# Kernel optimization log

Hardware: AMD Instinct MI355X
Metric: run time of the kernel (lower is better)

Reference implementation:

```python
import jax, jax.numpy as jnp
import numpy as np

DIM = 128
LAYER_GNN = 3
LAYER_CNN = 3
WINDOW = 11
K = 2 * WINDOW + 1  # conv kernel size 23
N_FP = 100000
N_WORD = 10000
N_ATOMS = 8192
L_PROT = 8192


def setup_inputs() -> dict:
    key = jax.random.key(0)
    ks = jax.random.split(key, 12)
    s = 0.1
    # sparse binary molecular adjacency (avg degree ~16), math is still dense matmul
    adjacency = (jax.random.uniform(ks[2], (N_ATOMS, N_ATOMS)) < 0.002).astype(jnp.float32)
    return {
        "fingerprints": jax.random.randint(ks[0], (N_ATOMS,), 0, N_FP),
        "words": jax.random.randint(ks[1], (L_PROT,), 0, N_WORD),
        "adjacency": adjacency,
        "emb_fp": jax.random.normal(ks[3], (N_FP, DIM), jnp.float32) * s,
        "emb_word": jax.random.normal(ks[4], (N_WORD, DIM), jnp.float32) * s,
        "Wg": jax.random.normal(ks[5], (LAYER_GNN, DIM, DIM), jnp.float32) * s,
        "bg": jnp.zeros((LAYER_GNN, DIM), jnp.float32),
        "conv_w": jax.random.normal(ks[6], (LAYER_CNN, 1, 1, K, K), jnp.float32) * s,
        "conv_b": jnp.zeros((LAYER_CNN,), jnp.float32),
        "Wa": jax.random.normal(ks[7], (DIM, DIM), jnp.float32) * s,
        "ba": jnp.zeros((DIM,), jnp.float32),
        "Wo": jax.random.normal(ks[8], (2, 2 * DIM), jnp.float32) * s,
        "bo": jnp.zeros((2,), jnp.float32),
    }


def reference(fingerprints, words, adjacency, emb_fp, emb_word, Wg, bg,
              conv_w, conv_b, Wa, ba, Wo, bo):
    # ---- GNN over compound graph ----
    xs = emb_fp[fingerprints]                      # [N_ATOMS, DIM]
    for i in range(LAYER_GNN):
        hs = jax.nn.relu(xs @ Wg[i].T + bg[i])     # Linear + ReLU
        xs = xs + adjacency @ hs                   # adjacency message passing
    x_compound = jnp.sum(xs, axis=0, keepdims=True)  # [1, DIM]

    # ---- attention-CNN over protein words ----
    xs_p = emb_word[words]                         # [L_PROT, DIM]
    x = x_compound                                 # [1, DIM]
    for i in range(LAYER_CNN):
        img = xs_p[None, None]                     # [1,1,L,DIM]
        h = jax.lax.conv_general_dilated(
            img, conv_w[i], window_strides=(1, 1),
            padding=[(WINDOW, WINDOW), (WINDOW, WINDOW)],
            dimension_numbers=("NCHW", "OIHW", "NCHW"))
        hs = jax.nn.relu(h[0, 0] + conv_b[i])      # [L, DIM]
        x = jax.nn.relu(x @ Wa.T + ba)             # [1, DIM]
        hs = jax.nn.relu(hs @ Wa.T + ba)           # [L, DIM]
        weights = jnp.tanh(x @ hs.T)               # [1, L]
        xs_p = weights.T * hs                      # [L, DIM]
    x_protein = jnp.sum(xs_p, axis=0, keepdims=True)  # [1, DIM]

    y = jnp.concatenate([x_compound, x_protein], axis=1)  # [1, 2*DIM]
    z = jax.nn.softmax(y @ Wo.T + bo, axis=1)
    return z[0]  # [2]
```

## Files before the change

kernel.cpp:

```cpp
#include <hip/hip_runtime.h>
#include <math.h>

#define DIM 128
#define NA 8192
#define CAP 64
#define NF (NA*DIM)

__global__ __launch_bounds__(256) void k_prep(
    const int* __restrict__ fp, const int* __restrict__ words,
    const float* __restrict__ emb_fp, const float* __restrict__ emb_w,
    const float* __restrict__ Wg, const float* __restrict__ Wa,
    float* __restrict__ xs, float* __restrict__ xsp,
    float* __restrict__ WgT, float* __restrict__ WaT,
    float* __restrict__ xc, float* __restrict__ xp,
    int* __restrict__ degcol, int* __restrict__ ctrs) {
  int b = blockIdx.x, tid = threadIdx.x;
  if (b < 1024) {
    int i = b * 256 + tid;
    int row = i >> 5, c4 = i & 31;
    ((float4*)(xs + (size_t)row * DIM))[c4] =
        ((const float4*)(emb_fp + (size_t)fp[row] * DIM))[c4];
  } else if (b < 2048) {
    int i = (b - 1024) * 256 + tid;
    int row = i >> 5, c4 = i & 31;
    ((float4*)(xsp + (size_t)row * DIM))[c4] =
        ((const float4*)(emb_w + (size_t)words[row] * DIM))[c4];
  } else if (b < 2112) {
    __shared__ float tile[32][33];
    int sub = b - 2048;
    int m = sub >> 4, t = sub & 15;
    int tx = t & 3, ty = t >> 2;
    const float* src = (m < 3) ? Wg + m * DIM * DIM : Wa;
    float*       dst = (m < 3) ? WgT + m * DIM * DIM : WaT;
    int x = tid & 31, y0 = tid >> 5;
    int xg = tx * 32 + x;
    for (int i = y0; i < 32; i += 8)
      tile[i][x] = src[(ty * 32 + i) * DIM + xg];
    __syncthreads();
    int xo = ty * 32 + x;
    for (int i = y0; i < 32; i += 8)
      dst[(tx * 32 + i) * DIM + xo] = tile[x][i];
  } else if (b == 2112) {
    if (tid < DIM) { xc[tid] = 0.f; xp[tid] = 0.f; }
    if (tid == 0) { ctrs[0] = 0; ctrs[1] = 0; }
  } else {
    int i = (b - 2113) * 256 + tid;
    int4 z; z.x = 0; z.y = 0; z.z = 0; z.w = 0;
    ((int4*)degcol)[i] = z;
  }
}

__global__ __launch_bounds__(512) void k_scan(
    const float* __restrict__ adj,
    const float* __restrict__ WgT, const float* __restrict__ bg,
    const float* __restrict__ xs, float* __restrict__ hs0,
    const float* __restrict__ xsp0, const float* __restrict__ cw,
    const float* __restrict__ cb, const float* __restrict__ WaT,
    const float* __restrict__ ba, float* __restrict__ hs2p0,
    int* __restrict__ ell, int* __restrict__ cnt, int* __restrict__ degcol) {
  __shared__ float U[54 * 156];
  __shared__ float wl[529];
  __shared__ float As[32 * 132];
  int b = blockIdx.x, tid = threadIdx.x;

  if (b < 256) {
    size_t rbase = (size_t)b * 32;
    for (int i = tid; i < 1024; i += 512) {
      int r = i >> 5, c = i & 31;
      *(float4*)&As[r * 132 + c * 4] = *(const float4*)&xs[(rbase + r) * DIM + c * 4];
    }
    __syncthreads();
    int rg = tid >> 5, j0 = (tid & 31) * 4;
    float acc[2][4];
    float4 b4 = *(const float4*)&bg[j0];
    acc[0][0] = acc[1][0] = b4.x; acc[0][1] = acc[1][1] = b4.y;
    acc[0][2] = acc[1][2] = b4.z; acc[0][3] = acc[1][3] = b4.w;
    for (int k4 = 0; k4 < 32; ++k4) {
      float a0[4], a1[4];
      *(float4*)a0 = *(float4*)&As[(rg * 2) * 132 + k4 * 4];
      *(float4*)a1 = *(float4*)&As[(rg * 2 + 1) * 132 + k4 * 4];
      #pragma unroll
      for (int kk = 0; kk < 4; ++kk) {
        float4 w4 = *(const float4*)&WgT[(k4 * 4 + kk) * DIM + j0];
        float w[4] = {w4.x, w4.y, w4.z, w4.w};
        #pragma unroll
        for (int c = 0; c < 4; ++c) {
          acc[0][c] += a0[kk] * w[c];
          acc[1][c] += a1[kk] * w[c];
        }
      }
    }
    #pragma unroll
    for (int rr = 0; rr < 2; ++rr) {
      float4 o;
      o.x = fmaxf(acc[rr][0], 0.f); o.y = fmaxf(acc[rr][1], 0.f);
      o.z = fmaxf(acc[rr][2], 0.f); o.w = fmaxf(acc[rr][3], 0.f);
      *(float4*)&hs0[(rbase + rg * 2 + rr) * DIM + j0] = o;
    }
  } else if (b < 512) {
    int blk = b - 256;
    int l0 = blk * 32;
    for (int i = tid; i < 529; i += 512) wl[i] = cw[i];
    for (int i = tid; i < 54 * 156; i += 512) {
      int ll = i / 156, dd = i % 156;
      int gl = l0 - 11 + ll, gd = dd - 11;
      float v = 0.f;
      if (gl >= 0 && gl < NA && (unsigned)gd < DIM)
        v = xsp0[(size_t)gl * DIM + gd];
      U[i] = v;
    }
    __syncthreads();
    {
      int ro = tid >> 4, d0 = (tid & 15) * 8;
      float a8[8];
      #pragma unroll
      for (int m = 0; m < 8; ++m) a8[m] = 0.f;
      for (int a = 0; a < 23; ++a) {
        float r[30];
        #pragma unroll
        for (int q = 0; q < 7; ++q)
          *(float4*)&r[4 * q] = *(const float4*)&U[(ro + a) * 156 + d0 + 4 * q];
        r[28] = U[(ro + a) * 156 + d0 + 28];
        r[29] = U[(ro + a) * 156 + d0 + 29];
        #pragma unroll
        for (int bb = 0; bb < 23; ++bb) {
          float wb = wl[a * 23 + bb];
          #pragma unroll
          for (int m = 0; m < 8; ++m) a8[m] += r[bb + m] * wb;
        }
      }
      float cbias = cb[0];
      #pragma unroll
      for (int m = 0; m < 8; ++m)
        As[ro * 132 + d0 + m] = fmaxf(a8[m] + cbias, 0.f);
    }
    __syncthreads();
    {
      int rg = tid >> 5, j0 = (tid & 31) * 4;
      float acc[2][4];
      float4 b4 = *(const float4*)&ba[j0];
      acc[0][0] = acc[1][0] = b4.x; acc[0][1] = acc[1][1] = b4.y;
      acc[0][2] = acc[1][2] = b4.z; acc[0][3] = acc[1][3] = b4.w;
      for (int k4 = 0; k4 < 32; ++k4) {
        float a0[4], a1[4];
        *(float4*)a0 = *(float4*)&As[(rg * 2) * 132 + k4 * 4];
        *(float4*)a1 = *(float4*)&As[(rg * 2 + 1) * 132 + k4 * 4];
        #pragma unroll
        for (int kk = 0; kk < 4; ++kk) {
          float4 w4 = *(const float4*)&WaT[(k4 * 4 + kk) * DIM + j0];
          float w[4] = {w4.x, w4.y, w4.z, w4.w};
          #pragma unroll
          for (int c = 0; c < 4; ++c) {
            acc[0][c] += a0[kk] * w[c];
            acc[1][c] += a1[kk] * w[c];
          }
        }
      }
      #pragma unroll
      for (int rr = 0; rr < 2; ++rr) {
        float4 o;
        o.x = fmaxf(acc[rr][0], 0.f); o.y = fmaxf(acc[rr][1], 0.f);
        o.z = fmaxf(acc[rr][2], 0.f); o.w = fmaxf(acc[rr][3], 0.f);
        *(float4*)&hs2p0[((size_t)l0 + rg * 2 + rr) * DIM + j0] = o;
      }
    }
  } else {
    int wv = tid >> 6, lane = tid & 63;
    int row = (b - 512) * 8 + wv;
    const float4* rp = (const float4*)(adj + (size_t)row * NA);
    int* er = ell + (size_t)row * CAP;
    int c = 0;
    float4 buf[8];
    #pragma unroll
    for (int u = 0; u < 8; ++u) buf[u] = rp[u * 64 + lane];
    for (int it = 0; it < 32; it += 8) {
      float4 nb[8];
      if (it + 8 < 32) {
        #pragma unroll
        for (int u = 0; u < 8; ++u) nb[u] = rp[(it + 8 + u) * 64 + lane];
      }
      #pragma unroll
      for (int u = 0; u < 8; ++u) {
        float f[4] = {buf[u].x, buf[u].y, buf[u].z, buf[u].w};
        #pragma unroll
        for (int j = 0; j < 4; ++j) {
          bool nz = (f[j] != 0.0f);
          unsigned long long m = __ballot(nz);
          if (nz) {
            int col = (it + u) * 256 + lane * 4 + j;
            int pos = c + __popcll(m & ((1ull << lane) - 1ull));
            if (pos < CAP) er[pos] = col;
            atomicAdd(&degcol[col], 1);
          }
          c += __popcll(m);
        }
      }
      #pragma unroll
      for (int u = 0; u < 8; ++u) buf[u] = nb[u];
    }
    if (lane == 0) cnt[row] = c > CAP ? CAP : c;
  }
}

__global__ __launch_bounds__(512) void k_gnn1(
    const int* __restrict__ ell, const int* __restrict__ cnt,
    const float* __restrict__ hs0, float* __restrict__ xs,
    const float* __restrict__ WgT1, const float* __restrict__ bg1,
    float* __restrict__ hs1) {
  __shared__ float As[16 * 132];
  int tid = threadIdx.x;
  int wv = tid >> 6, lane = tid & 63;
  size_t rbase = (size_t)blockIdx.x * 16;
  for (int rr = 0; rr < 2; ++rr) {
    int lr = wv * 2 + rr;
    size_t row = rbase + lr;
    int n = cnt[row];
    const int* er = ell + row * CAP;
    float2 a2 = *(const float2*)&xs[row * DIM + lane * 2];
    int t = 0;
    for (; t + 4 <= n; t += 4) {
      int j0 = er[t], j1 = er[t + 1], j2 = er[t + 2], j3 = er[t + 3];
      float2 h0 = *(const float2*)&hs0[(size_t)j0 * DIM + lane * 2];
      float2 h1 = *(const float2*)&hs0[(size_t)j1 * DIM + lane * 2];
      float2 h2 = *(const float2*)&hs0[(size_t)j2 * DIM + lane * 2];
      float2 h3 = *(const float2*)&hs0[(size_t)j3 * DIM + lane * 2];
      a2.x += (h0.x + h1.x) + (h2.x + h3.x);
      a2.y += (h0.y + h1.y) + (h2.y + h3.y);
    }
    for (; t < n; ++t) {
      float2 h = *(const float2*)&hs0[(size_t)er[t] * DIM + lane * 2];
      a2.x += h.x; a2.y += h.y;
    }
    *(float2*)&xs[row * DIM + lane * 2] = a2;
    As[lr * 132 + lane * 2] = a2.x;
    As[lr * 132 + lane * 2 + 1] = a2.y;
  }
  __syncthreads();
  int rg = tid >> 5, j0 = (tid & 31) * 4;
  float acc[4];
  float4 b4 = *(const float4*)&bg1[j0];
  acc[0] = b4.x; acc[1] = b4.y; acc[2] = b4.z; acc[3] = b4.w;
  for (int k4 = 0; k4 < 32; ++k4) {
    float a[4];
    *(float4*)a = *(float4*)&As[rg * 132 + k4 * 4];
    #pragma unroll
    for (int kk = 0; kk < 4; ++kk) {
      float4 w4 = *(const float4*)&WgT1[(k4 * 4 + kk) * DIM + j0];
      acc[0] += a[kk] * w4.x; acc[1] += a[kk] * w4.y;
      acc[2] += a[kk] * w4.z; acc[3] += a[kk] * w4.w;
    }
  }
  float4 o;
  o.x = fmaxf(acc[0], 0.f); o.y = fmaxf(acc[1], 0.f);
  o.z = fmaxf(acc[2], 0.f); o.w = fmaxf(acc[3], 0.f);
  *(float4*)&hs1[(rbase + rg) * DIM + j0] = o;
}

__global__ __launch_bounds__(512) void k_gnn2(
    const int* __restrict__ ell, const int* __restrict__ cnt,
    const float* __restrict__ hs1, const float* __restrict__ xs,
    const float* __restrict__ WgT2, const float* __restrict__ bg2,
    const int* __restrict__ degcol, float* __restrict__ xc,
    const float* __restrict__ WaT, const float* __restrict__ ba,
    float* __restrict__ xall, int* __restrict__ ctr) {
  __shared__ float As[16 * 132];
  __shared__ float H2[16 * 132];
  __shared__ float red[4 * DIM];
  __shared__ float xb[DIM];
  __shared__ int lastf;
  int tid = threadIdx.x;
  int wv = tid >> 6, lane = tid & 63;
  size_t rbase = (size_t)blockIdx.x * 16;
  for (int rr = 0; rr < 2; ++rr) {
    int lr = wv * 2 + rr;
    size_t row = rbase + lr;
    int n = cnt[row];
    const int* er = ell + row * CAP;
    float2 a2 = *(const float2*)&xs[row * DIM + lane * 2];
    int t = 0;
    for (; t + 4 <= n; t += 4) {
      int j0 = er[t], j1 = er[t + 1], j2 = er[t + 2], j3 = er[t + 3];
      float2 h0 = *(const float2*)&hs1[(size_t)j0 * DIM + lane * 2];
      float2 h1 = *(const float2*)&hs1[(size_t)j1 * DIM + lane * 2];
      float2 h2 = *(const float2*)&hs1[(size_t)j2 * DIM + lane * 2];
      float2 h3 = *(const float2*)&hs1[(size_t)j3 * DIM + lane * 2];
      a2.x += (h0.x + h1.x) + (h2.x + h3.x);
      a2.y += (h0.y + h1.y) + (h2.y + h3.y);
    }
    for (; t < n; ++t) {
      float2 h = *(const float2*)&hs1[(size_t)er[t] * DIM + lane * 2];
      a2.x += h.x; a2.y += h.y;
    }
    As[lr * 132 + lane * 2] = a2.x;
    As[lr * 132 + lane * 2 + 1] = a2.y;
  }
  __syncthreads();
  {
    int rg = tid >> 5, j0 = (tid & 31) * 4;
    float acc[4];
    float4 b4 = *(const float4*)&bg2[j0];
    acc[0] = b4.x; acc[1] = b4.y; acc[2] = b4.z; acc[3] = b4.w;
    for (int k4 = 0; k4 < 32; ++k4) {
      float a[4];
      *(float4*)a = *(float4*)&As[rg * 132 + k4 * 4];
      #pragma unroll
      for (int kk = 0; kk < 4; ++kk) {
        float4 w4 = *(const float4*)&WgT2[(k4 * 4 + kk) * DIM + j0];
        acc[0] += a[kk] * w4.x; acc[1] += a[kk] * w4.y;
        acc[2] += a[kk] * w4.z; acc[3] += a[kk] * w4.w;
      }
    }
    H2[rg * 132 + j0]     = fmaxf(acc[0], 0.f);
    H2[rg * 132 + j0 + 1] = fmaxf(acc[1], 0.f);
    H2[rg * 132 + j0 + 2] = fmaxf(acc[2], 0.f);
    H2[rg * 132 + j0 + 3] = fmaxf(acc[3], 0.f);
  }
  __syncthreads();
  {
    int c = tid & 127, h = tid >> 7;
    float s = 0.f;
    #pragma unroll
    for (int q = 0; q < 4; ++q) {
      int r = h + q * 4;
      float dg = (float)degcol[rbase + r];
      s += As[r * 132 + c] + dg * H2[r * 132 + c];
    }
    red[h * DIM + c] = s;
    __syncthreads();
    if (h == 0)
      atomicAdd(&xc[c], red[c] + red[DIM + c] + red[2 * DIM + c] + red[3 * DIM + c]);
  }
  __threadfence();
  __syncthreads();
  if (tid == 0) lastf = (atomicAdd(ctr, 1) == (int)gridDim.x - 1);
  __syncthreads();
  if (lastf) {
    __threadfence();
    if (tid < DIM) xb[tid] = atomicAdd(&xc[tid], 0.0f);
    __syncthreads();
    for (int i = 0; i < 3; ++i) {
      float a = 0.f;
      if (tid < DIM) {
        a = ba[tid];
        for (int k = 0; k < DIM; ++k) a += xb[k] * WaT[k * DIM + tid];
        a = fmaxf(a, 0.f);
      }
      __syncthreads();
      if (tid < DIM) { xb[tid] = a; xall[i * DIM + tid] = a; }
      __syncthreads();
    }
  }
}

__global__ __launch_bounds__(512) void k_prot1(
    const float* __restrict__ hs2p0, const float* __restrict__ xall,
    const float* __restrict__ cw1, const float* __restrict__ cb1,
    const float* __restrict__ WaT, const float* __restrict__ ba,
    float* __restrict__ hs2p1) {
  __shared__ float U[54 * 156];
  __shared__ float wl[529];
  __shared__ float As[32 * 132];
  __shared__ float w54[56];
  __shared__ float xrow[DIM];
  int tid = threadIdx.x;
  int wv = tid >> 6, lane = tid & 63;
  int l0 = blockIdx.x * 32;
  for (int i = tid; i < 529; i += 512) wl[i] = cw1[i];
  if (tid < DIM) xrow[tid] = xall[tid];
  for (int i = tid; i < 54 * 156; i += 512) {
    int ll = i / 156, dd = i % 156;
    int gl = l0 - 11 + ll, gd = dd - 11;
    float v = 0.f;
    if (gl >= 0 && gl < NA && (unsigned)gd < DIM)
      v = hs2p0[(size_t)gl * DIM + gd];
    U[i] = v;
  }
  __syncthreads();
  for (int ll = wv; ll < 54; ll += 8) {
    float p = U[ll * 156 + 11 + lane * 2] * xrow[lane * 2]
            + U[ll * 156 + 12 + lane * 2] * xrow[lane * 2 + 1];
    #pragma unroll
    for (int s = 32; s > 0; s >>= 1) p += __shfl_xor(p, s, 64);
    if (lane == 0) w54[ll] = tanhf(p);
  }
  __syncthreads();
  for (int i = tid; i < 54 * 128; i += 512) {
    int ll = i >> 7, dd = i & 127;
    U[ll * 156 + 11 + dd] *= w54[ll];
  }
  __syncthreads();
  {
    int ro = tid >> 4, d0 = (tid & 15) * 8;
    float a8[8];
    #pragma unroll
    for (int m = 0; m < 8; ++m) a8[m] = 0.f;
    for (int a = 0; a < 23; ++a) {
      float r[30];
      #pragma unroll
      for (int q = 0; q < 7; ++q)
        *(float4*)&r[4 * q] = *(const float4*)&U[(ro + a) * 156 + d0 + 4 * q];
      r[28] = U[(ro + a) * 156 + d0 + 28];
      r[29] = U[(ro + a) * 156 + d0 + 29];
      #pragma unroll
      for (int bb = 0; bb < 23; ++bb) {
        float wb = wl[a * 23 + bb];
        #pragma unroll
        for (int m = 0; m < 8; ++m) a8[m] += r[bb + m] * wb;
      }
    }
    float cbias = cb1[0];
    #pragma unroll
    for (int m = 0; m < 8; ++m)
      As[ro * 132 + d0 + m] = fmaxf(a8[m] + cbias, 0.f);
  }
  __syncthreads();
  {
    int rg = tid >> 5, j0 = (tid & 31) * 4;
    float acc[2][4];
    float4 b4 = *(const float4*)&ba[j0];
    acc[0][0] = acc[1][0] = b4.x; acc[0][1] = acc[1][1] = b4.y;
    acc[0][2] = acc[1][2] = b4.z; acc[0][3] = acc[1][3] = b4.w;
    for (int k4 = 0; k4 < 32; ++k4) {
      float a0[4], a1[4];
      *(float4*)a0 = *(float4*)&As[(rg * 2) * 132 + k4 * 4];
      *(float4*)a1 = *(float4*)&As[(rg * 2 + 1) * 132 + k4 * 4];
      #pragma unroll
      for (int kk = 0; kk < 4; ++kk) {
        float4 w4 = *(const float4*)&WaT[(k4 * 4 + kk) * DIM + j0];
        float w[4] = {w4.x, w4.y, w4.z, w4.w};
        #pragma unroll
        for (int c = 0; c < 4; ++c) {
          acc[0][c] += a0[kk] * w[c];
          acc[1][c] += a1[kk] * w[c];
        }
      }
    }
    #pragma unroll
    for (int rr = 0; rr < 2; ++rr) {
      float4 o;
      o.x = fmaxf(acc[rr][0], 0.f); o.y = fmaxf(acc[rr][1], 0.f);
      o.z = fmaxf(acc[rr][2], 0.f); o.w = fmaxf(acc[rr][3], 0.f);
      *(float4*)&hs2p1[((size_t)l0 + rg * 2 + rr) * DIM + j0] = o;
    }
  }
}

__global__ __launch_bounds__(512) void k_prot2(
    const float* __restrict__ hs2p1, const float* __restrict__ xall,
    const float* __restrict__ cw2, const float* __restrict__ cb2,
    const float* __restrict__ WaT, const float* __restrict__ ba,
    float* __restrict__ xp, const float* __restrict__ xc,
    const float* __restrict__ Wo, const float* __restrict__ bo,
    float* __restrict__ out, int* __restrict__ ctr) {
  __shared__ float U[54 * 156];
  __shared__ float wl[529];
  __shared__ float As[32 * 132];
  __shared__ float w54[56];
  __shared__ float xrow[DIM];
  __shared__ float red[4 * DIM];
  __shared__ float fs[32];
  __shared__ int lastf;
  int tid = threadIdx.x;
  int wv = tid >> 6, lane = tid & 63;
  int l0 = blockIdx.x * 32;
  float* H2 = U;

  for (int i = tid; i < 529; i += 512) wl[i] = cw2[i];
  if (tid < DIM) xrow[tid] = xall[DIM + tid];
  for (int i = tid; i < 54 * 156; i += 512) {
    int ll = i / 156, dd = i % 156;
    int gl = l0 - 11 + ll, gd = dd - 11;
    float v = 0.f;
    if (gl >= 0 && gl < NA && (unsigned)gd < DIM)
      v = hs2p1[(size_t)gl * DIM + gd];
    U[i] = v;
  }
  __syncthreads();
  for (int ll = wv; ll < 54; ll += 8) {
    float p = U[ll * 156 + 11 + lane * 2] * xrow[lane * 2]
            + U[ll * 156 + 12 + lane * 2] * xrow[lane * 2 + 1];
    #pragma unroll
    for (int s = 32; s > 0; s >>= 1) p += __shfl_xor(p, s, 64);
    if (lane == 0) w54[ll] = tanhf(p);
  }
  __syncthreads();
  for (int i = tid; i < 54 * 128; i += 512) {
    int ll = i >> 7, dd = i & 127;
    U[ll * 156 + 11 + dd] *= w54[ll];
  }
  __syncthreads();
  {
    int ro = tid >> 4, d0 = (tid & 15) * 8;
    float a8[8];
    #pragma unroll
    for (int m = 0; m < 8; ++m) a8[m] = 0.f;
    for (int a = 0; a < 23; ++a) {
      float r[30];
      #pragma unroll
      for (int q = 0; q < 7; ++q)
        *(float4*)&r[4 * q] = *(const float4*)&U[(ro + a) * 156 + d0 + 4 * q];
      r[28] = U[(ro + a) * 156 + d0 + 28];
      r[29] = U[(ro + a) * 156 + d0 + 29];
      #pragma unroll
      for (int bb = 0; bb < 23; ++bb) {
        float wb = wl[a * 23 + bb];
        #pragma unroll
        for (int m = 0; m < 8; ++m) a8[m] += r[bb + m] * wb;
      }
    }
    float cbias = cb2[0];
    #pragma unroll
    for (int m = 0; m < 8; ++m)
      As[ro * 132 + d0 + m] = fmaxf(a8[m] + cbias, 0.f);
  }
  __syncthreads();
  {
    int rg = tid >> 5, j0 = (tid & 31) * 4;
    float acc[2][4];
    float4 b4 = *(const float4*)&ba[j0];
    acc[0][0] = acc[1][0] = b4.x; acc[0][1] = acc[1][1] = b4.y;
    acc[0][2] = acc[1][2] = b4.z; acc[0][3] = acc[1][3] = b4.w;
    for (int k4 = 0; k4 < 32; ++k4) {
      float a0[4], a1[4];
      *(float4*)a0 = *(float4*)&As[(rg * 2) * 132 + k4 * 4];
      *(float4*)a1 = *(float4*)&As[(rg * 2 + 1) * 132 + k4 * 4];
      #pragma unroll
      for (int kk = 0; kk < 4; ++kk) {
        float4 w4 = *(const float4*)&WaT[(k4 * 4 + kk) * DIM + j0];
        float w[4] = {w4.x, w4.y, w4.z, w4.w};
        #pragma unroll
        for (int c = 0; c < 4; ++c) {
          acc[0][c] += a0[kk] * w[c];
          acc[1][c] += a1[kk] * w[c];
        }
      }
    }
    #pragma unroll
    for (int rr = 0; rr < 2; ++rr) {
      H2[(rg * 2 + rr) * 132 + j0]     = fmaxf(acc[rr][0], 0.f);
      H2[(rg * 2 + rr) * 132 + j0 + 1] = fmaxf(acc[rr][1], 0.f);
      H2[(rg * 2 + rr) * 132 + j0 + 2] = fmaxf(acc[rr][2], 0.f);
      H2[(rg * 2 + rr) * 132 + j0 + 3] = fmaxf(acc[rr][3], 0.f);
    }
  }
  __syncthreads();
  {
    float x0 = xall[2 * DIM + lane * 2], x1 = xall[2 * DIM + lane * 2 + 1];
    for (int rr = 0; rr < 4; ++rr) {
      int row = wv * 4 + rr;
      float2 h = *(float2*)&H2[row * 132 + lane * 2];
      float p = h.x * x0 + h.y * x1;
      #pragma unroll
      for (int s = 32; s > 0; s >>= 1) p += __shfl_xor(p, s, 64);
      if (lane == 0) w54[row] = tanhf(p);
    }
  }
  __syncthreads();
  {
    int c = tid & 127, h = tid >> 7;
    float s = 0.f;
    #pragma unroll
    for (int q = 0; q < 8; ++q) {
      int r = h + q * 4;
      s += w54[r] * H2[r * 132 + c];
    }
    red[h * DIM + c] = s;
    __syncthreads();
    if (h == 0)
      atomicAdd(&xp[c], red[c] + red[DIM + c] + red[2 * DIM + c] + red[3 * DIM + c]);
  }
  __threadfence();
  __syncthreads();
  if (tid == 0) lastf = (atomicAdd(ctr, 1) == (int)gridDim.x - 1);
  __syncthreads();
  if (lastf) {
    __threadfence();
    float p0 = 0.f, p1 = 0.f;
    if (tid < 256) {
      float y = (tid < DIM) ? xc[tid] : atomicAdd(&xp[tid - DIM], 0.0f);
      p0 = y * Wo[tid];
      p1 = y * Wo[256 + tid];
    }
    #pragma unroll
    for (int s = 32; s > 0; s >>= 1) {
      p0 += __shfl_xor(p0, s, 64);
      p1 += __shfl_xor(p1, s, 64);
    }
    if (tid < 256 && lane == 0) { fs[wv] = p0; fs[16 + wv] = p1; }
    __syncthreads();
    if (tid == 0) {
      float l0v = bo[0], l1v = bo[1];
      #pragma unroll
      for (int w = 0; w < 4; ++w) { l0v += fs[w]; l1v += fs[16 + w]; }
      float m = fmaxf(l0v, l1v);
      float e0 = expf(l0v - m), e1 = expf(l1v - m);
      out[0] = e0 / (e0 + e1);
      out[1] = e1 / (e0 + e1);
    }
  }
}

extern "C" void kernel_launch(void* const* d_in, const int* in_sizes, int n_in,
                              void* d_out, int out_size, void* d_ws, size_t ws_size,
                              hipStream_t stream) {
  const int*   fp     = (const int*)d_in[0];
  const int*   words  = (const int*)d_in[1];
  const float* adj    = (const float*)d_in[2];
  const float* emb_fp = (const float*)d_in[3];
  const float* emb_w  = (const float*)d_in[4];
  const float* Wg     = (const float*)d_in[5];
  const float* bg     = (const float*)d_in[6];
  const float* cw     = (const float*)d_in[7];
  const float* cb     = (const float*)d_in[8];
  const float* Wa     = (const float*)d_in[9];
  const float* ba     = (const float*)d_in[10];
  const float* Wo     = (const float*)d_in[11];
  const float* bo     = (const float*)d_in[12];
  float* out = (float*)d_out;

  float* ws    = (float*)d_ws;
  float* xs    = ws;
  float* bufB  = ws + (size_t)NF;
  float* bufC  = ws + 2 * (size_t)NF;
  float* bufD  = ws + 3 * (size_t)NF;
  int*   ell   = (int*)(ws + 4 * (size_t)NF);
  int*   cnt   = ell + (size_t)NA * CAP;
  int*   degcol= cnt + NA;
  float* xc    = (float*)(degcol + NA);
  float* xp    = xc + DIM;
  float* xall  = xp + DIM;
  float* WgT   = xall + 3 * DIM;
  float* WaT   = WgT + 3 * DIM * DIM;
  int*   ctrs  = (int*)(WaT + DIM * DIM);

  k_prep<<<dim3(2121), 256, 0, stream>>>(fp, words, emb_fp, emb_w, Wg, Wa,
                                         xs, bufC, WgT, WaT, xc, xp, degcol, ctrs);
  k_scan<<<dim3(1536), 512, 0, stream>>>(adj, WgT, bg, xs, bufB,
                                         bufC, cw, cb, WaT, ba, bufD,
                                         ell, cnt, degcol);
  k_gnn1<<<dim3(512), 512, 0, stream>>>(ell, cnt, bufB, xs,
                                        WgT + (size_t)DIM * DIM, bg + DIM, bufC);
  k_gnn2<<<dim3(512), 512, 0, stream>>>(ell, cnt, bufC, xs,
                                        WgT + 2 * (size_t)DIM * DIM, bg + 2 * DIM,
                                        degcol, xc, WaT, ba, xall, ctrs);
  k_prot1<<<dim3(256), 512, 0, stream>>>(bufD, xall, cw + 529, cb + 1,
                                         WaT, ba, bufB);
  k_prot2<<<dim3(256), 512, 0, stream>>>(bufB, xall, cw + 2 * 529, cb + 2,
                                         WaT, ba, xp, xc, Wo, bo, out, ctrs + 1);
}
```

Before: 304.4 us.

## Split adjacency scan into own kernel, stage weights in LDS, replace atomics with partials

The fused scan kernel is split into a standalone ELL-build kernel and a separate heads kernel. The GEMM helpers now stage the weight matrix in shared memory in two halves instead of reading it from global memory per thread. The GNN kernels use 8 rows per block over 1024 blocks. Float atomics into xc/xp are replaced by per-block partial sums that the last block reduces. This aims to cut global weight traffic and atomic contention and to make the final reduction deterministic, at the cost of an extra launch and the loss of overlap between the adjacency scan and the head GEMMs.

```diff
diff --git a/kernel.cpp b/kernel.cpp
--- a/kernel.cpp
+++ b/kernel.cpp
@@ -5,6 +5,130 @@
 #define NA 8192
 #define CAP 64
 #define NF (NA*DIM)
+
+
+__device__ __forceinline__ void d_gemm32(int tid, const float* As, float* Ws,
+    const float* __restrict__ W, const float* __restrict__ bias,
+    float* __restrict__ out, int ostr, size_t obase) {
+  int rg = tid >> 5, j0 = (tid & 31) * 4;
+  float acc[2][4];
+  float4 b4 = *(const float4*)&bias[j0];
+  #pragma unroll
+  for (int rr = 0; rr < 2; ++rr) {
+    acc[rr][0] = b4.x; acc[rr][1] = b4.y; acc[rr][2] = b4.z; acc[rr][3] = b4.w;
+  }
+  #pragma unroll
+  for (int half = 0; half < 2; ++half) {
+    __syncthreads();
+    for (int i = tid; i < 2048; i += 512)
+      ((float4*)Ws)[i] = ((const float4*)(W + half * 64 * DIM))[i];
+    __syncthreads();
+    for (int k4 = 0; k4 < 16; ++k4) {
+      float a0[4], a1[4];
+      *(float4*)a0 = *(const float4*)&As[(rg * 2) * 132 + half * 64 + k4 * 4];
+      *(float4*)a1 = *(const float4*)&As[(rg * 2 + 1) * 132 + half * 64 + k4 * 4];
+      #pragma unroll
+      for (int kk = 0; kk < 4; ++kk) {
+        float4 w4 = *(const float4*)&Ws[(k4 * 4 + kk) * DIM + j0];
+        float w[4] = {w4.x, w4.y, w4.z, w4.w};
+        #pragma unroll
+        for (int c = 0; c < 4; ++c) {
+          acc[0][c] += a0[kk] * w[c];
+          acc[1][c] += a1[kk] * w[c];
+        }
+      }
+    }
+  }
+  #pragma unroll
+  for (int rr = 0; rr < 2; ++rr) {
+    float4 o;
+    o.x = fmaxf(acc[rr][0], 0.f); o.y = fmaxf(acc[rr][1], 0.f);
+    o.z = fmaxf(acc[rr][2], 0.f); o.w = fmaxf(acc[rr][3], 0.f);
+    *(float4*)&out[(obase + rg * 2 + rr) * (size_t)ostr + j0] = o;
+  }
+}
+
+__device__ __forceinline__ void d_conv512(int tid, const float* U, const float* wl,
+                                          float cbias, float* Ao) {
+  int ro = tid >> 4, d0 = (tid & 15) * 8;
+  float a8[8];
+  #pragma unroll
+  for (int m = 0; m < 8; ++m) a8[m] = 0.f;
+  for (int a = 0; a < 23; ++a) {
+    float r[30];
+    #pragma unroll
+    for (int q = 0; q < 7; ++q)
+      *(float4*)&r[4 * q] = *(const float4*)&U[(ro + a) * 156 + d0 + 4 * q];
+    r[28] = U[(ro + a) * 156 + d0 + 28];
+    r[29] = U[(ro + a) * 156 + d0 + 29];
+    #pragma unroll
+    for (int bb = 0; bb < 23; ++bb) {
+      float wb = wl[a * 23 + bb];
+      #pragma unroll
+      for (int m = 0; m < 8; ++m) a8[m] += r[bb + m] * wb;
+    }
+  }
+  #pragma unroll
+  for (int m = 0; m < 8; ++m)
+    Ao[ro * 132 + d0 + m] = fmaxf(a8[m] + cbias, 0.f);
+}
+
+__device__ __forceinline__ void d_tile512(int blk, int tid, const float* __restrict__ src,
+                                          const float* __restrict__ cwl,
+                                          float* U, float* wl) {
+  for (int i = tid; i < 529; i += 512) wl[i] = cwl[i];
+  int l0 = blk * 32;
+  for (int i = tid; i < 54 * 156; i += 512) {
+    int ll = i / 156, dd = i % 156;
+    int gl = l0 - 11 + ll, gd = dd - 11;
+    float v = 0.f;
+    if (gl >= 0 && gl < NA && (unsigned)gd < DIM)
+      v = src[(size_t)gl * DIM + gd];
+    U[i] = v;
+  }
+}
+
+__device__ __forceinline__ void d_halo_attn(int tid, float* U, const float* xrow,
+                                            float* w54) {
+  int wv = tid >> 6, lane = tid & 63;
+  for (int ll = wv; ll < 54; ll += 8) {
+    float p = U[ll * 156 + 11 + lane * 2] * xrow[lane * 2]
+            + U[ll * 156 + 12 + lane * 2] * xrow[lane * 2 + 1];
+    #pragma unroll
+    for (int s = 32; s > 0; s >>= 1) p += __shfl_xor(p, s, 64);
+    if (lane == 0) w54[ll] = tanhf(p);
+  }
+  __syncthreads();
+  for (int i = tid; i < 54 * 128; i += 512) {
+    int ll = i >> 7, dd = i & 127;
+    U[ll * 156 + 11 + dd] *= w54[ll];
+  }
+}
+
+__device__ __forceinline__ void d_spmv_row(size_t row, int lane,
+    const int* __restrict__ ell, const int* __restrict__ cnt,
+    const float* __restrict__ hs, float* __restrict__ xs, float* AsRow, int wb) {
+  int n = cnt[row];
+  const int* er = ell + row * CAP;
+  float2 a2 = *(const float2*)&xs[row * DIM + lane * 2];
+  int t = 0;
+  for (; t + 4 <= n; t += 4) {
+    int j0 = er[t], j1 = er[t + 1], j2 = er[t + 2], j3 = er[t + 3];
+    float2 h0 = *(const float2*)&hs[(size_t)j0 * DIM + lane * 2];
+    float2 h1 = *(const float2*)&hs[(size_t)j1 * DIM + lane * 2];
+    float2 h2 = *(const float2*)&hs[(size_t)j2 * DIM + lane * 2];
+    float2 h3 = *(const float2*)&hs[(size_t)j3 * DIM + lane * 2];
+    a2.x += (h0.x + h1.x) + (h2.x + h3.x);
+    a2.y += (h0.y + h1.y) + (h2.y + h3.y);
+  }
+  for (; t < n; ++t) {
+    float2 h = *(const float2*)&hs[(size_t)er[t] * DIM + lane * 2];
+    a2.x += h.x; a2.y += h.y;
+  }
+  if (wb) *(float2*)&xs[row * DIM + lane * 2] = a2;
+  AsRow[lane * 2] = a2.x;
+  AsRow[lane * 2 + 1] = a2.y;
+}
 
 __global__ __launch_bounds__(256) void k_prep(
     const int* __restrict__ fp, const int* __restrict__ words,
@@ -12,7 +136,6 @@
     const float* __restrict__ Wg, const float* __restrict__ Wa,
     float* __restrict__ xs, float* __restrict__ xsp,
     float* __restrict__ WgT, float* __restrict__ WaT,
-    float* __restrict__ xc, float* __restrict__ xp,
     int* __restrict__ degcol, int* __restrict__ ctrs) {
   int b = blockIdx.x, tid = threadIdx.x;
   if (b < 1024) {
@@ -40,295 +163,158 @@
     int xo = ty * 32 + x;
     for (int i = y0; i < 32; i += 8)
       dst[(tx * 32 + i) * DIM + xo] = tile[x][i];
-  } else if (b == 2112) {
-    if (tid < DIM) { xc[tid] = 0.f; xp[tid] = 0.f; }
-    if (tid == 0) { ctrs[0] = 0; ctrs[1] = 0; }
-  } else {
-    int i = (b - 2113) * 256 + tid;
+  } else if (b < 2120) {
+    int i = (b - 2112) * 256 + tid;
     int4 z; z.x = 0; z.y = 0; z.z = 0; z.w = 0;
     ((int4*)degcol)[i] = z;
-  }
-}
-
-__global__ __launch_bounds__(512) void k_scan(
-    const float* __restrict__ adj,
-    const float* __restrict__ WgT, const float* __restrict__ bg,
-    const float* __restrict__ xs, float* __restrict__ hs0,
-    const float* __restrict__ xsp0, const float* __restrict__ cw,
-    const float* __restrict__ cb, const float* __restrict__ WaT,
-    const float* __restrict__ ba, float* __restrict__ hs2p0,
-    int* __restrict__ ell, int* __restrict__ cnt, int* __restrict__ degcol) {
-  __shared__ float U[54 * 156];
-  __shared__ float wl[529];
-  __shared__ float As[32 * 132];
+  } else {
+    if (tid == 0) { ctrs[0] = 0; ctrs[1] = 0; }
+  }
+}
+
+__global__ __launch_bounds__(256) void k_ell(const float* __restrict__ adj,
+                                             int* __restrict__ ell, int* __restrict__ cnt,
+                                             int* __restrict__ degcol) {
+  int wv = threadIdx.x >> 6, lane = threadIdx.x & 63;
+  int row = blockIdx.x * 4 + wv;
+  const float4* rp = (const float4*)(adj + (size_t)row * NA);
+  int* er = ell + (size_t)row * CAP;
+  int c = 0;
+  float4 buf[8];
+  #pragma unroll
+  for (int u = 0; u < 8; ++u) buf[u] = rp[u * 64 + lane];
+  for (int it = 0; it < 32; it += 8) {
+    float4 nb[8];
+    if (it + 8 < 32) {
+      #pragma unroll
+      for (int u = 0; u < 8; ++u) nb[u] = rp[(it + 8 + u) * 64 + lane];
+    }
+    #pragma unroll
+    for (int u = 0; u < 8; ++u) {
+      float f[4] = {buf[u].x, buf[u].y, buf[u].z, buf[u].w};
+      #pragma unroll
+      for (int j = 0; j < 4; ++j) {
+        bool nz = (f[j] != 0.0f);
+        unsigned long long m = __ballot(nz);
+        if (nz) {
+          int col = (it + u) * 256 + lane * 4 + j;
+          int pos = c + __popcll(m & ((1ull << lane) - 1ull));
+          if (pos < CAP) er[pos] = col;
+          atomicAdd(&degcol[col], 1);
+        }
+        c += __popcll(m);
+      }
+    }
+    #pragma unroll
+    for (int u = 0; u < 8; ++u) buf[u] = nb[u];
+  }
+  if (lane == 0) cnt[row] = c > CAP ? CAP : c;
+}
+
+__global__ __launch_bounds__(512) void k_heads(
+    const float* __restrict__ xs, const float* __restrict__ WgT0,
+    const float* __restrict__ bg0, float* __restrict__ hs0,
+    const float* __restrict__ xsp0, const float* __restrict__ cw0,
+    const float* __restrict__ cb0, const float* __restrict__ WaT,
+    const float* __restrict__ ba, float* __restrict__ hs2p0) {
+  __shared__ float S[13184];
   int b = blockIdx.x, tid = threadIdx.x;
-
   if (b < 256) {
+    float* As = S;
+    float* Ws = S + 4224;
     size_t rbase = (size_t)b * 32;
     for (int i = tid; i < 1024; i += 512) {
       int r = i >> 5, c = i & 31;
       *(float4*)&As[r * 132 + c * 4] = *(const float4*)&xs[(rbase + r) * DIM + c * 4];
     }
-    __syncthreads();
-    int rg = tid >> 5, j0 = (tid & 31) * 4;
-    float acc[2][4];
-    float4 b4 = *(const float4*)&bg[j0];
-    acc[0][0] = acc[1][0] = b4.x; acc[0][1] = acc[1][1] = b4.y;
-    acc[0][2] = acc[1][2] = b4.z; acc[0][3] = acc[1][3] = b4.w;
-    for (int k4 = 0; k4 < 32; ++k4) {
-      float a0[4], a1[4];
-      *(float4*)a0 = *(float4*)&As[(rg * 2) * 132 + k4 * 4];
-      *(float4*)a1 = *(float4*)&As[(rg * 2 + 1) * 132 + k4 * 4];
-      #pragma unroll
-      for (int kk = 0; kk < 4; ++kk) {
-        float4 w4 = *(const float4*)&WgT[(k4 * 4 + kk) * DIM + j0];
-        float w[4] = {w4.x, w4.y, w4.z, w4.w};
-        #pragma unroll
-        for (int c = 0; c < 4; ++c) {
-          acc[0][c] += a0[kk] * w[c];
-          acc[1][c] += a1[kk] * w[c];
-        }
-      }
-    }
-    #pragma unroll
-    for (int rr = 0; rr < 2; ++rr) {
-      float4 o;
-      o.x = fmaxf(acc[rr][0], 0.f); o.y = fmaxf(acc[rr][1], 0.f);
-      o.z = fmaxf(acc[rr][2], 0.f); o.w = fmaxf(acc[rr][3], 0.f);
-      *(float4*)&hs0[(rbase + rg * 2 + rr) * DIM + j0] = o;
-    }
-  } else if (b < 512) {
+    d_gemm32(tid, As, Ws, WgT0, bg0, hs0, DIM, rbase);
+  } else {
     int blk = b - 256;
-    int l0 = blk * 32;
-    for (int i = tid; i < 529; i += 512) wl[i] = cw[i];
-    for (int i = tid; i < 54 * 156; i += 512) {
-      int ll = i / 156, dd = i % 156;
-      int gl = l0 - 11 + ll, gd = dd - 11;
-      float v = 0.f;
-      if (gl >= 0 && gl < NA && (unsigned)gd < DIM)
-        v = xsp0[(size_t)gl * DIM + gd];
-      U[i] = v;
-    }
-    __syncthreads();
-    {
-      int ro = tid >> 4, d0 = (tid & 15) * 8;
-      float a8[8];
-      #pragma unroll
-      for (int m = 0; m < 8; ++m) a8[m] = 0.f;
-      for (int a = 0; a < 23; ++a) {
-        float r[30];
-        #pragma unroll
-        for (int q = 0; q < 7; ++q)
-          *(float4*)&r[4 * q] = *(const float4*)&U[(ro + a) * 156 + d0 + 4 * q];
-        r[28] = U[(ro + a) * 156 + d0 + 28];
-        r[29] = U[(ro + a) * 156 + d0 + 29];
-        #pragma unroll
-        for (int bb = 0; bb < 23; ++bb) {
-          float wb = wl[a * 23 + bb];
-          #pragma unroll
-          for (int m = 0; m < 8; ++m) a8[m] += r[bb + m] * wb;
-        }
-      }
-      float cbias = cb[0];
-      #pragma unroll
-      for (int m = 0; m < 8; ++m)
-        As[ro * 132 + d0 + m] = fmaxf(a8[m] + cbias, 0.f);
-    }
-    __syncthreads();
-    {
-      int rg = tid >> 5, j0 = (tid & 31) * 4;
-      float acc[2][4];
-      float4 b4 = *(const float4*)&ba[j0];
-      acc[0][0] = acc[1][0] = b4.x; acc[0][1] = acc[1][1] = b4.y;
-      acc[0][2] = acc[1][2] = b4.z; acc[0][3] = acc[1][3] = b4.w;
-      for (int k4 = 0; k4 < 32; ++k4) {
-        float a0[4], a1[4];
-        *(float4*)a0 = *(float4*)&As[(rg * 2) * 132 + k4 * 4];
-        *(float4*)a1 = *(float4*)&As[(rg * 2 + 1) * 132 + k4 * 4];
-        #pragma unroll
-        for (int kk = 0; kk < 4; ++kk) {
-          float4 w4 = *(const float4*)&WaT[(k4 * 4 + kk) * DIM + j0];
-          float w[4] = {w4.x, w4.y, w4.z, w4.w};
-          #pragma unroll
-          for (int c = 0; c < 4; ++c) {
-            acc[0][c] += a0[kk] * w[c];
-            acc[1][c] += a1[kk] * w[c];
-          }
-        }
-      }
-      #pragma unroll
-      for (int rr = 0; rr < 2; ++rr) {
-        float4 o;
-        o.x = fmaxf(acc[rr][0], 0.f); o.y = fmaxf(acc[rr][1], 0.f);
-        o.z = fmaxf(acc[rr][2], 0.f); o.w = fmaxf(acc[rr][3], 0.f);
-        *(float4*)&hs2p0[((size_t)l0 + rg * 2 + rr) * DIM + j0] = o;
-      }
-    }
-  } else {
-    int wv = tid >> 6, lane = tid & 63;
-    int row = (b - 512) * 8 + wv;
-    const float4* rp = (const float4*)(adj + (size_t)row * NA);
-    int* er = ell + (size_t)row * CAP;
-    int c = 0;
-    float4 buf[8];
-    #pragma unroll
-    for (int u = 0; u < 8; ++u) buf[u] = rp[u * 64 + lane];
-    for (int it = 0; it < 32; it += 8) {
-      float4 nb[8];
-      if (it + 8 < 32) {
-        #pragma unroll
-        for (int u = 0; u < 8; ++u) nb[u] = rp[(it + 8 + u) * 64 + lane];
-      }
-      #pragma unroll
-      for (int u = 0; u < 8; ++u) {
-        float f[4] = {buf[u].x, buf[u].y, buf[u].z, buf[u].w};
-        #pragma unroll
-        for (int j = 0; j < 4; ++j) {
-          bool nz = (f[j] != 0.0f);
-          unsigned long long m = __ballot(nz);
-          if (nz) {
-            int col = (it + u) * 256 + lane * 4 + j;
-            int pos = c + __popcll(m & ((1ull << lane) - 1ull));
-            if (pos < CAP) er[pos] = col;
-            atomicAdd(&degcol[col], 1);
-          }
-          c += __popcll(m);
-        }
-      }
-      #pragma unroll
-      for (int u = 0; u < 8; ++u) buf[u] = nb[u];
-    }
-    if (lane == 0) cnt[row] = c > CAP ? CAP : c;
-  }
-}
-
-__global__ __launch_bounds__(512) void k_gnn1(
+    float* U  = S;
+    float* wl = S + 8424;
+    float* Ao = S + 8960;
+    d_tile512(blk, tid, xsp0, cw0, U, wl);
+    __syncthreads();
+    d_conv512(tid, U, wl, cb0[0], Ao);
+    d_gemm32(tid, Ao, U, WaT, ba, hs2p0, DIM, (size_t)blk * 32);
+  }
+}
+
+__global__ __launch_bounds__(512) void k_g1(
     const int* __restrict__ ell, const int* __restrict__ cnt,
     const float* __restrict__ hs0, float* __restrict__ xs,
     const float* __restrict__ WgT1, const float* __restrict__ bg1,
     float* __restrict__ hs1) {
-  __shared__ float As[16 * 132];
+  __shared__ float As[8 * 132];
+  __shared__ float Ws[64 * 128];
   int tid = threadIdx.x;
   int wv = tid >> 6, lane = tid & 63;
-  size_t rbase = (size_t)blockIdx.x * 16;
-  for (int rr = 0; rr < 2; ++rr) {
-    int lr = wv * 2 + rr;
-    size_t row = rbase + lr;
-    int n = cnt[row];
-    const int* er = ell + row * CAP;
-    float2 a2 = *(const float2*)&xs[row * DIM + lane * 2];
-    int t = 0;
-    for (; t + 4 <= n; t += 4) {
-      int j0 = er[t], j1 = er[t + 1], j2 = er[t + 2], j3 = er[t + 3];
-      float2 h0 = *(const float2*)&hs0[(size_t)j0 * DIM + lane * 2];
-      float2 h1 = *(const float2*)&hs0[(size_t)j1 * DIM + lane * 2];
-      float2 h2 = *(const float2*)&hs0[(size_t)j2 * DIM + lane * 2];
-      float2 h3 = *(const float2*)&hs0[(size_t)j3 * DIM + lane * 2];
-      a2.x += (h0.x + h1.x) + (h2.x + h3.x);
-      a2.y += (h0.y + h1.y) + (h2.y + h3.y);
-    }
-    for (; t < n; ++t) {
-      float2 h = *(const float2*)&hs0[(size_t)er[t] * DIM + lane * 2];
-      a2.x += h.x; a2.y += h.y;
-    }
-    *(float2*)&xs[row * DIM + lane * 2] = a2;
-    As[lr * 132 + lane * 2] = a2.x;
-    As[lr * 132 + lane * 2 + 1] = a2.y;
-  }
-  __syncthreads();
-  int rg = tid >> 5, j0 = (tid & 31) * 4;
-  float acc[4];
-  float4 b4 = *(const float4*)&bg1[j0];
-  acc[0] = b4.x; acc[1] = b4.y; acc[2] = b4.z; acc[3] = b4.w;
-  for (int k4 = 0; k4 < 32; ++k4) {
-    float a[4];
-    *(float4*)a = *(float4*)&As[rg * 132 + k4 * 4];
-    #pragma unroll
-    for (int kk = 0; kk < 4; ++kk) {
-      float4 w4 = *(const float4*)&WgT1[(k4 * 4 + kk) * DIM + j0];
-      acc[0] += a[kk] * w4.x; acc[1] += a[kk] * w4.y;
-      acc[2] += a[kk] * w4.z; acc[3] += a[kk] * w4.w;
-    }
-  }
-  float4 o;
-  o.x = fmaxf(acc[0], 0.f); o.y = fmaxf(acc[1], 0.f);
-  o.z = fmaxf(acc[2], 0.f); o.w = fmaxf(acc[3], 0.f);
-  *(float4*)&hs1[(rbase + rg) * DIM + j0] = o;
-}
-
-__global__ __launch_bounds__(512) void k_gnn2(
+  size_t rbase = (size_t)blockIdx.x * 8;
+  d_spmv_row(rbase + wv, lane, ell, cnt, hs0, xs, &As[wv * 132], 1);
+  int c0 = lane * 2;
+  float acc0 = bg1[c0], acc1 = bg1[c0 + 1];
+  #pragma unroll
+  for (int half = 0; half < 2; ++half) {
+    __syncthreads();
+    for (int i = tid; i < 2048; i += 512)
+      ((float4*)Ws)[i] = ((const float4*)(WgT1 + half * 64 * DIM))[i];
+    __syncthreads();
+    for (int k = 0; k < 64; ++k) {
+      float av = As[wv * 132 + half * 64 + k];
+      float2 w2 = *(const float2*)&Ws[k * DIM + c0];
+      acc0 += av * w2.x;
+      acc1 += av * w2.y;
+    }
+  }
+  float2 o;
+  o.x = fmaxf(acc0, 0.f); o.y = fmaxf(acc1, 0.f);
+  *(float2*)&hs1[(rbase + wv) * DIM + c0] = o;
+}
+
+__global__ __launch_bounds__(512) void k_g2(
     const int* __restrict__ ell, const int* __restrict__ cnt,
     const float* __restrict__ hs1, const float* __restrict__ xs,
     const float* __restrict__ WgT2, const float* __restrict__ bg2,
-    const int* __restrict__ degcol, float* __restrict__ xc,
-    const float* __restrict__ WaT, const float* __restrict__ ba,
-    float* __restrict__ xall, int* __restrict__ ctr) {
-  __shared__ float As[16 * 132];
-  __shared__ float H2[16 * 132];
+    const int* __restrict__ degcol, float* __restrict__ partialG,
+    float* __restrict__ xc, const float* __restrict__ WaT,
+    const float* __restrict__ ba, float* __restrict__ xall,
+    int* __restrict__ ctr) {
+  __shared__ float As[8 * 132];
+  __shared__ float H2[8 * 132];
+  __shared__ float Ws[64 * 128];
   __shared__ float red[4 * DIM];
   __shared__ float xb[DIM];
   __shared__ int lastf;
   int tid = threadIdx.x;
   int wv = tid >> 6, lane = tid & 63;
-  size_t rbase = (size_t)blockIdx.x * 16;
-  for (int rr = 0; rr < 2; ++rr) {
-    int lr = wv * 2 + rr;
-    size_t row = rbase + lr;
-    int n = cnt[row];
-    const int* er = ell + row * CAP;
-    float2 a2 = *(const float2*)&xs[row * DIM + lane * 2];
-    int t = 0;
-    for (; t + 4 <= n; t += 4) {
-      int j0 = er[t], j1 = er[t + 1], j2 = er[t + 2], j3 = er[t + 3];
-      float2 h0 = *(const float2*)&hs1[(size_t)j0 * DIM + lane * 2];
-      float2 h1 = *(const float2*)&hs1[(size_t)j1 * DIM + lane * 2];
-      float2 h2 = *(const float2*)&hs1[(size_t)j2 * DIM + lane * 2];
-      float2 h3 = *(const float2*)&hs1[(size_t)j3 * DIM + lane * 2];
-      a2.x += (h0.x + h1.x) + (h2.x + h3.x);
-      a2.y += (h0.y + h1.y) + (h2.y + h3.y);
-    }
-    for (; t < n; ++t) {
-      float2 h = *(const float2*)&hs1[(size_t)er[t] * DIM + lane * 2];
-      a2.x += h.x; a2.y += h.y;
-    }
-    As[lr * 132 + lane * 2] = a2.x;
-    As[lr * 132 + lane * 2 + 1] = a2.y;
-  }
-  __syncthreads();
-  {
-    int rg = tid >> 5, j0 = (tid & 31) * 4;
-    float acc[4];
-    float4 b4 = *(const float4*)&bg2[j0];
-    acc[0] = b4.x; acc[1] = b4.y; acc[2] = b4.z; acc[3] = b4.w;
-    for (int k4 = 0; k4 < 32; ++k4) {
-      float a[4];
-      *(float4*)a = *(float4*)&As[rg * 132 + k4 * 4];
-      #pragma unroll
-      for (int kk = 0; kk < 4; ++kk) {
-        float4 w4 = *(const float4*)&WgT2[(k4 * 4 + kk) * DIM + j0];
-        acc[0] += a[kk] * w4.x; acc[1] += a[kk] * w4.y;
-        acc[2] += a[kk] * w4.z; acc[3] += a[kk] * w4.w;
-      }
-    }
-    H2[rg * 132 + j0]     = fmaxf(acc[0], 0.f);
-    H2[rg * 132 + j0 + 1] = fmaxf(acc[1], 0.f);
-    H2[rg * 132 + j0 + 2] = fmaxf(acc[2], 0.f);
-    H2[rg * 132 + j0 + 3] = fmaxf(acc[3], 0.f);
-  }
-  __syncthreads();
-  {
-    int c = tid & 127, h = tid >> 7;
+  size_t rbase = (size_t)blockIdx.x * 8;
+  d_spmv_row(rbase + wv, lane, ell, cnt, hs1, (float*)xs, &As[wv * 132], 0);
+  int c0 = lane * 2;
+  float acc0 = bg2[c0], acc1 = bg2[c0 + 1];
+  #pragma unroll
+  for (int half = 0; half < 2; ++half) {
+    __syncthreads();
+    for (int i = tid; i < 2048; i += 512)
+      ((float4*)Ws)[i] = ((const float4*)(WgT2 + half * 64 * DIM))[i];
+    __syncthreads();
+    for (int k = 0; k < 64; ++k) {
+      float av = As[wv * 132 + half * 64 + k];
+      float2 w2 = *(const float2*)&Ws[k * DIM + c0];
+      acc0 += av * w2.x;
+      acc1 += av * w2.y;
+    }
+  }
+  H2[wv * 132 + c0]     = fmaxf(acc0, 0.f);
+  H2[wv * 132 + c0 + 1] = fmaxf(acc1, 0.f);
+  __syncthreads();
+  if (tid < DIM) {
     float s = 0.f;
     #pragma unroll
-    for (int q = 0; q < 4; ++q) {
-      int r = h + q * 4;
+    for (int r = 0; r < 8; ++r) {
       float dg = (float)degcol[rbase + r];
-      s += As[r * 132 + c] + dg * H2[r * 132 + c];
-    }
-    red[h * DIM + c] = s;
-    __syncthreads();
-    if (h == 0)
-      atomicAdd(&xc[c], red[c] + red[DIM + c] + red[2 * DIM + c] + red[3 * DIM + c]);
+      s += As[r * 132 + tid] + dg * H2[r * 132 + tid];
+    }
+    partialG[blockIdx.x * DIM + tid] = s;
   }
   __threadfence();
   __syncthreads();
@@ -336,7 +322,21 @@
   __syncthreads();
   if (lastf) {
     __threadfence();
-    if (tid < DIM) xb[tid] = atomicAdd(&xc[tid], 0.0f);
+    {
+      int c = tid & 127, q = tid >> 7;
+      float s = 0.f;
+      for (int bb = q * 256; bb < q * 256 + 256; bb += 4) {
+        s += partialG[(bb + 0) * DIM + c] + partialG[(bb + 1) * DIM + c]
+           + partialG[(bb + 2) * DIM + c] + partialG[(bb + 3) * DIM + c];
+      }
+      red[q * DIM + c] = s;
+    }
+    __syncthreads();
+    if (tid < DIM) {
+      float v = red[tid] + red[DIM + tid] + red[2 * DIM + tid] + red[3 * DIM + tid];
+      xc[tid] = v;
+      xb[tid] = v;
+    }
     __syncthreads();
     for (int i = 0; i < 3; ++i) {
       float a = 0.f;
@@ -352,203 +352,58 @@
   }
 }
 
-__global__ __launch_bounds__(512) void k_prot1(
+__global__ __launch_bounds__(512) void k_p1(
     const float* __restrict__ hs2p0, const float* __restrict__ xall,
     const float* __restrict__ cw1, const float* __restrict__ cb1,
     const float* __restrict__ WaT, const float* __restrict__ ba,
     float* __restrict__ hs2p1) {
   __shared__ float U[54 * 156];
   __shared__ float wl[529];
-  __shared__ float As[32 * 132];
+  __shared__ float Ao[32 * 132];
   __shared__ float w54[56];
   __shared__ float xrow[DIM];
-  int tid = threadIdx.x;
-  int wv = tid >> 6, lane = tid & 63;
-  int l0 = blockIdx.x * 32;
-  for (int i = tid; i < 529; i += 512) wl[i] = cw1[i];
+  int tid = threadIdx.x, blk = blockIdx.x;
   if (tid < DIM) xrow[tid] = xall[tid];
-  for (int i = tid; i < 54 * 156; i += 512) {
-    int ll = i / 156, dd = i % 156;
-    int gl = l0 - 11 + ll, gd = dd - 11;
-    float v = 0.f;
-    if (gl >= 0 && gl < NA && (unsigned)gd < DIM)
-      v = hs2p0[(size_t)gl * DIM + gd];
-    U[i] = v;
-  }
-  __syncthreads();
-  for (int ll = wv; ll < 54; ll += 8) {
-    float p = U[ll * 156 + 11 + lane * 2] * xrow[lane * 2]
-            + U[ll * 156 + 12 + lane * 2] * xrow[lane * 2 + 1];
-    #pragma unroll
-    for (int s = 32; s > 0; s >>= 1) p += __shfl_xor(p, s, 64);
-    if (lane == 0) w54[ll] = tanhf(p);
-  }
-  __syncthreads();
-  for (int i = tid; i < 54 * 128; i += 512) {
-    int ll = i >> 7, dd = i & 127;
-    U[ll * 156 + 11 + dd] *= w54[ll];
-  }
-  __syncthreads();
-  {
-    int ro = tid >> 4, d0 = (tid & 15) * 8;
-    float a8[8];
-    #pragma unroll
-    for (int m = 0; m < 8; ++m) a8[m] = 0.f;
-    for (int a = 0; a < 23; ++a) {
-      float r[30];
-      #pragma unroll
-      for (int q = 0; q < 7; ++q)
-        *(float4*)&r[4 * q] = *(const float4*)&U[(ro + a) * 156 + d0 + 4 * q];
-      r[28] = U[(ro + a) * 156 + d0 + 28];
-      r[29] = U[(ro + a) * 156 + d0 + 29];
-      #pragma unroll
-      for (int bb = 0; bb < 23; ++bb) {
-        float wb = wl[a * 23 + bb];
-        #pragma unroll
-        for (int m = 0; m < 8; ++m) a8[m] += r[bb + m] * wb;
-      }
-    }
-    float cbias = cb1[0];
-    #pragma unroll
-    for (int m = 0; m < 8; ++m)
-      As[ro * 132 + d0 + m] = fmaxf(a8[m] + cbias, 0.f);
-  }
-  __syncthreads();
-  {
-    int rg = tid >> 5, j0 = (tid & 31) * 4;
-    float acc[2][4];
-    float4 b4 = *(const float4*)&ba[j0];
-    acc[0][0] = acc[1][0] = b4.x; acc[0][1] = acc[1][1] = b4.y;
-    acc[0][2] = acc[1][2] = b4.z; acc[0][3] = acc[1][3] = b4.w;
-    for (int k4 = 0; k4 < 32; ++k4) {
-      float a0[4], a1[4];
-      *(float4*)a0 = *(float4*)&As[(rg * 2) * 132 + k4 * 4];
-      *(float4*)a1 = *(float4*)&As[(rg * 2 + 1) * 132 + k4 * 4];
-      #pragma unroll
-      for (int kk = 0; kk < 4; ++kk) {
-        float4 w4 = *(const float4*)&WaT[(k4 * 4 + kk) * DIM + j0];
-        float w[4] = {w4.x, w4.y, w4.z, w4.w};
-        #pragma unroll
-        for (int c = 0; c < 4; ++c) {
-          acc[0][c] += a0[kk] * w[c];
-          acc[1][c] += a1[kk] * w[c];
-        }
-      }
-    }
-    #pragma unroll
-    for (int rr = 0; rr < 2; ++rr) {
-      float4 o;
-      o.x = fmaxf(acc[rr][0], 0.f); o.y = fmaxf(acc[rr][1], 0.f);
-      o.z = fmaxf(acc[rr][2], 0.f); o.w = fmaxf(acc[rr][3], 0.f);
-      *(float4*)&hs2p1[((size_t)l0 + rg * 2 + rr) * DIM + j0] = o;
-    }
-  }
-}
-
-__global__ __launch_bounds__(512) void k_prot2(
+  d_tile512(blk, tid, hs2p0, cw1, U, wl);
+  __syncthreads();
+  d_halo_attn(tid, U, xrow, w54);
+  __syncthreads();
+  d_conv512(tid, U, wl, cb1[0], Ao);
+  d_gemm32(tid, Ao, U, WaT, ba, hs2p1, DIM, (size_t)blk * 32);
+}
+
+__global__ __launch_bounds__(512) void k_p2(
     const float* __restrict__ hs2p1, const float* __restrict__ xall,
     const float* __restrict__ cw2, const float* __restrict__ cb2,
     const float* __restrict__ WaT, const float* __restrict__ ba,
-    float* __restrict__ xp, const float* __restrict__ xc,
+    float* __restrict__ partialP, const float* __restrict__ xc,
     const float* __restrict__ Wo, const float* __restrict__ bo,
     float* __restrict__ out, int* __restrict__ ctr) {
   __shared__ float U[54 * 156];
   __shared__ float wl[529];
-  __shared__ float As[32 * 132];
+  __shared__ float Ao[32 * 132];
+  __shared__ float H2[32 * 132];
   __shared__ float w54[56];
   __shared__ float xrow[DIM];
   __shared__ float red[4 * DIM];
+  __shared__ float xps[DIM];
   __shared__ float fs[32];
   __shared__ int lastf;
-  int tid = threadIdx.x;
+  int tid = threadIdx.x, blk = blockIdx.x;
   int wv = tid >> 6, lane = tid & 63;
-  int l0 = blockIdx.x * 32;
-  float* H2 = U;
-
-  for (int i = tid; i < 529; i += 512) wl[i] = cw2[i];
   if (tid < DIM) xrow[tid] = xall[DIM + tid];
-  for (int i = tid; i < 54 * 156; i += 512) {
-    int ll = i / 156, dd = i % 156;
-    int gl = l0 - 11 + ll, gd = dd - 11;
-    float v = 0.f;
-    if (gl >= 0 && gl < NA && (unsigned)gd < DIM)
-      v = hs2p1[(size_t)gl * DIM + gd];
-    U[i] = v;
-  }
-  __syncthreads();
-  for (int ll = wv; ll < 54; ll += 8) {
-    float p = U[ll * 156 + 11 + lane * 2] * xrow[lane * 2]
-            + U[ll * 156 + 12 + lane * 2] * xrow[lane * 2 + 1];
-    #pragma unroll
-    for (int s = 32; s > 0; s >>= 1) p += __shfl_xor(p, s, 64);
-    if (lane == 0) w54[ll] = tanhf(p);
-  }
-  __syncthreads();
-  for (int i = tid; i < 54 * 128; i += 512) {
-    int ll = i >> 7, dd = i & 127;
-    U[ll * 156 + 11 + dd] *= w54[ll];
-  }
-  __syncthreads();
-  {
-    int ro = tid >> 4, d0 = (tid & 15) * 8;
-    float a8[8];
-    #pragma unroll
-    for (int m = 0; m < 8; ++m) a8[m] = 0.f;
-    for (int a = 0; a < 23; ++a) {
-      float r[30];
-      #pragma unroll
-      for (int q = 0; q < 7; ++q)
-        *(float4*)&r[4 * q] = *(const float4*)&U[(ro + a) * 156 + d0 + 4 * q];
-      r[28] = U[(ro + a) * 156 + d0 + 28];
-      r[29] = U[(ro + a) * 156 + d0 + 29];
-      #pragma unroll
-      for (int bb = 0; bb < 23; ++bb) {
-        float wb = wl[a * 23 + bb];
-        #pragma unroll
-        for (int m = 0; m < 8; ++m) a8[m] += r[bb + m] * wb;
-      }
-    }
-    float cbias = cb2[0];
-    #pragma unroll
-    for (int m = 0; m < 8; ++m)
-      As[ro * 132 + d0 + m] = fmaxf(a8[m] + cbias, 0.f);
-  }
-  __syncthreads();
-  {
-    int rg = tid >> 5, j0 = (tid & 31) * 4;
-    float acc[2][4];
-    float4 b4 = *(const float4*)&ba[j0];
-    acc[0][0] = acc[1][0] = b4.x; acc[0][1] = acc[1][1] = b4.y;
-    acc[0][2] = acc[1][2] = b4.z; acc[0][3] = acc[1][3] = b4.w;
-    for (int k4 = 0; k4 < 32; ++k4) {
-      float a0[4], a1[4];
-      *(float4*)a0 = *(float4*)&As[(rg * 2) * 132 + k4 * 4];
-      *(float4*)a1 = *(float4*)&As[(rg * 2 + 1) * 132 + k4 * 4];
-      #pragma unroll
-      for (int kk = 0; kk < 4; ++kk) {
-        float4 w4 = *(const float4*)&WaT[(k4 * 4 + kk) * DIM + j0];
-        float w[4] = {w4.x, w4.y, w4.z, w4.w};
-        #pragma unroll
-        for (int c = 0; c < 4; ++c) {
-          acc[0][c] += a0[kk] * w[c];
-          acc[1][c] += a1[kk] * w[c];
-        }
-      }
-    }
-    #pragma unroll
-    for (int rr = 0; rr < 2; ++rr) {
-      H2[(rg * 2 + rr) * 132 + j0]     = fmaxf(acc[rr][0], 0.f);
-      H2[(rg * 2 + rr) * 132 + j0 + 1] = fmaxf(acc[rr][1], 0.f);
-      H2[(rg * 2 + rr) * 132 + j0 + 2] = fmaxf(acc[rr][2], 0.f);
-      H2[(rg * 2 + rr) * 132 + j0 + 3] = fmaxf(acc[rr][3], 0.f);
-    }
-  }
+  d_tile512(blk, tid, hs2p1, cw2, U, wl);
+  __syncthreads();
+  d_halo_attn(tid, U, xrow, w54);
+  __syncthreads();
+  d_conv512(tid, U, wl, cb2[0], Ao);
+  d_gemm32(tid, Ao, U, WaT, ba, H2, 132, 0);
   __syncthreads();
   {
     float x0 = xall[2 * DIM + lane * 2], x1 = xall[2 * DIM + lane * 2 + 1];
     for (int rr = 0; rr < 4; ++rr) {
       int row = wv * 4 + rr;
-      float2 h = *(float2*)&H2[row * 132 + lane * 2];
+      float2 h = *(const float2*)&H2[row * 132 + lane * 2];
       float p = h.x * x0 + h.y * x1;
       #pragma unroll
       for (int s = 32; s > 0; s >>= 1) p += __shfl_xor(p, s, 64);
@@ -556,18 +411,11 @@
     }
   }
   __syncthreads();
-  {
-    int c = tid & 127, h = tid >> 7;
+  if (tid < DIM) {
     float s = 0.f;
     #pragma unroll
-    for (int q = 0; q < 8; ++q) {
-      int r = h + q * 4;
-      s += w54[r] * H2[r * 132 + c];
-    }
-    red[h * DIM + c] = s;
-    __syncthreads();
-    if (h == 0)
-      atomicAdd(&xp[c], red[c] + red[DIM + c] + red[2 * DIM + c] + red[3 * DIM + c]);
+    for (int r = 0; r < 32; ++r) s += w54[r] * H2[r * 132 + tid];
+    partialP[blk * DIM + tid] = s;
   }
   __threadfence();
   __syncthreads();
@@ -575,9 +423,22 @@
   __syncthreads();
   if (lastf) {
     __threadfence();
+    {
+      int c = tid & 127, q = tid >> 7;
+      float s = 0.f;
+      for (int bb = q * 64; bb < q * 64 + 64; bb += 4) {
+        s += partialP[(bb + 0) * DIM + c] + partialP[(bb + 1) * DIM + c]
+           + partialP[(bb + 2) * DIM + c] + partialP[(bb + 3) * DIM + c];
+      }
+      red[q * DIM + c] = s;
+    }
+    __syncthreads();
+    if (tid < DIM)
+      xps[tid] = red[tid] + red[DIM + tid] + red[2 * DIM + tid] + red[3 * DIM + tid];
+    __syncthreads();
     float p0 = 0.f, p1 = 0.f;
     if (tid < 256) {
-      float y = (tid < DIM) ? xc[tid] : atomicAdd(&xp[tid - DIM], 0.0f);
+      float y = (tid < DIM) ? xc[tid] : xps[tid - DIM];
       p0 = y * Wo[tid];
       p1 = y * Wo[256 + tid];
     }
@@ -589,11 +450,11 @@
     if (tid < 256 && lane == 0) { fs[wv] = p0; fs[16 + wv] = p1; }
     __syncthreads();
     if (tid == 0) {
-      float l0v = bo[0], l1v = bo[1];
+      float l0 = bo[0], l1 = bo[1];
       #pragma unroll
-      for (int w = 0; w < 4; ++w) { l0v += fs[w]; l1v += fs[16 + w]; }
-      float m = fmaxf(l0v, l1v);
-      float e0 = expf(l0v - m), e1 = expf(l1v - m);
+      for (int w = 0; w < 4; ++w) { l0 += fs[w]; l1 += fs[16 + w]; }
+      float m = fmaxf(l0, l1);
+      float e0 = expf(l0 - m), e1 = expf(l1 - m);
       out[0] = e0 / (e0 + e1);
       out[1] = e1 / (e0 + e1);
     }
@@ -626,25 +487,25 @@
   int*   ell   = (int*)(ws + 4 * (size_t)NF);
   int*   cnt   = ell + (size_t)NA * CAP;
   int*   degcol= cnt + NA;
-  float* xc    = (float*)(degcol + NA);
-  float* xp    = xc + DIM;
-  float* xall  = xp + DIM;
+  int*   ctrs  = degcol + NA;
+  float* xc    = (float*)(ctrs + 2);
+  float* xall  = xc + DIM;
   float* WgT   = xall + 3 * DIM;
   float* WaT   = WgT + 3 * DIM * DIM;
-  int*   ctrs  = (int*)(WaT + DIM * DIM);
+  float* partG = WaT + DIM * DIM;
+  float* partP = partG + 1024 * DIM;
 
   k_prep<<<dim3(2121), 256, 0, stream>>>(fp, words, emb_fp, emb_w, Wg, Wa,
-                                         xs, bufC, WgT, WaT, xc, xp, degcol, ctrs);
-  k_scan<<<dim3(1536), 512, 0, stream>>>(adj, WgT, bg, xs, bufB,
-                                         bufC, cw, cb, WaT, ba, bufD,
-                                         ell, cnt, degcol);
-  k_gnn1<<<dim3(512), 512, 0, stream>>>(ell, cnt, bufB, xs,
-                                        WgT + (size_t)DIM * DIM, bg + DIM, bufC);
-  k_gnn2<<<dim3(512), 512, 0, stream>>>(ell, cnt, bufC, xs,
-                                        WgT + 2 * (size_t)DIM * DIM, bg + 2 * DIM,
-                                        degcol, xc, WaT, ba, xall, ctrs);
-  k_prot1<<<dim3(256), 512, 0, stream>>>(bufD, xall, cw + 529, cb + 1,
-                                         WaT, ba, bufB);
-  k_prot2<<<dim3(256), 512, 0, stream>>>(bufB, xall, cw + 2 * 529, cb + 2,
-                                         WaT, ba, xp, xc, Wo, bo, out, ctrs + 1);
-}
+                                         xs, bufC, WgT, WaT, degcol, ctrs);
+  k_ell<<<dim3(NA / 4), 256, 0, stream>>>(adj, ell, cnt, degcol);
+  k_heads<<<dim3(512), 512, 0, stream>>>(xs, WgT, bg, bufB,
+                                         bufC, cw, cb, WaT, ba, bufD);
+  k_g1<<<dim3(1024), 512, 0, stream>>>(ell, cnt, bufB, xs,
+                                       WgT + (size_t)DIM * DIM, bg + DIM, bufC);
+  k_g2<<<dim3(1024), 512, 0, stream>>>(ell, cnt, bufC, xs,
+                                       WgT + 2 * (size_t)DIM * DIM, bg + 2 * DIM,
+                                       degcol, partG, xc, WaT, ba, xall, ctrs);
+  k_p1<<<dim3(256), 512, 0, stream>>>(bufD, xall, cw + 529, cb + 1, WaT, ba, bufB);
+  k_p2<<<dim3(256), 512, 0, stream>>>(bufB, xall, cw + 2 * 529, cb + 2, WaT, ba,
+                                      partP, xc, Wo, bo, out, ctrs + 1);
+}
```

Result: slower. 518.8 us (+70.4%).
